# Kernel optimization log

Hardware: AMD Instinct MI355X
Metric: run time of the kernel (lower is better)

## Reference

```python
import jax, jax.numpy as jnp
import numpy as np

N_NODES = 50000
N_EDGES = 800000
DIM = 256


def setup_inputs() -> dict:
    key = jax.random.key(0)
    k1, k2, k3, k4 = jax.random.split(key, 4)
    x = jax.random.normal(k1, (N_NODES, DIM), dtype=jnp.float32)
    edge_index = jax.random.randint(k2, (2, N_EDGES), 0, N_NODES, dtype=jnp.int64)
    # GCNConv learned params (glorot-style weight, zero bias like PyG default init)
    W = jax.random.normal(k3, (DIM, DIM), dtype=jnp.float32) * (1.0 / np.sqrt(DIM))
    b = jnp.zeros((DIM,), dtype=jnp.float32)
    return {"x": x, "edge_index": edge_index, "W": W, "b": b}


def reference(x, edge_index, W, b):
    # GNNBlock forward (eval mode: dropout is identity; normalizer=Identity,
    # activation=ReLU, projection=Identity since in_dim==out_dim).
    n = x.shape[0]
    # --- GCNConv with self-loops and symmetric normalization ---
    loop = jnp.arange(n, dtype=edge_index.dtype)
    src = jnp.concatenate([edge_index[0], loop])  # [E+N]
    dst = jnp.concatenate([edge_index[1], loop])  # [E+N]
    ones = jnp.ones(src.shape[0], dtype=x.dtype)
    deg = jax.ops.segment_sum(ones, dst, num_segments=n)  # in-degree incl. self-loop
    dinv = jnp.where(deg > 0, jax.lax.rsqrt(deg), 0.0)
    norm = dinv[src] * dinv[dst]  # [E+N]
    h = x @ W  # transform first (in->out), then aggregate
    msg = h[src] * norm[:, None]  # gather + scale, [E+N, DIM]
    agg = jax.ops.segment_sum(msg, dst, num_segments=n) + b  # scatter-add
    # --- norm (Identity) -> activation (ReLU) -> residual -> dropout (eval) ---
    out = jax.nn.relu(agg) + x
    return out
```

## Files before the change

### kernel.cpp

```cpp
#include <hip/hip_runtime.h>

#define N_NODES 50000
#define DIM 256
#define NBUCK 196
#define BCAP 6144
#define CEDGES 2048
#define MSTRIDE 512
#define APAD 264
#define EPAD 260
#define TROWS 16

typedef __attribute__((ext_vector_type(8))) short bf16x8;
typedef __attribute__((ext_vector_type(4))) float f32x4;
typedef __attribute__((ext_vector_type(2))) float f32x2;
union U16 { uint4 u; bf16x8 s; };

__device__ __forceinline__ unsigned short f2b(float f) {
    unsigned int u = __float_as_uint(f);
    return (unsigned short)((u + 0x7FFFu + ((u >> 16) & 1u)) >> 16);
}

__global__ __launch_bounds__(256) void prep_bin_kernel(const int* __restrict__ src,
                                                       const int* __restrict__ dst, int E,
                                                       int nCoarse,
                                                       unsigned int* __restrict__ slab2,
                                                       int* __restrict__ meta_t,
                                                       const float* __restrict__ W,
                                                       uint4* __restrict__ Bpack,
                                                       const float* __restrict__ x,
                                                       unsigned int* __restrict__ xq) {
    __shared__ int hist[NBUCK];
    __shared__ int scn[NBUCK];
    __shared__ int cur[NBUCK];
    __shared__ int s2[256];
    __shared__ unsigned int sorted[CEDGES];

    const int tid = threadIdx.x;

    if (blockIdx.x >= (unsigned)nCoarse) {
        int role = blockIdx.x - nCoarse;
        if (role < 32) {
            int gid  = role * 256 + tid;
            int lane = gid & 63;
            int u    = (gid >> 6) & 15;
            int ki   = gid >> 10;
            int n    = u * 16 + (lane & 15);
            int k0   = ki * 32 + (lane >> 4) * 8;
            unsigned int w[4];
            #pragma unroll
            for (int p = 0; p < 4; ++p) {
                unsigned int lo = f2b(W[(size_t)(k0 + 2 * p) * DIM + n]);
                unsigned int hi = f2b(W[(size_t)(k0 + 2 * p + 1) * DIM + n]);
                w[p] = lo | (hi << 16);
            }
            Bpack[gid] = make_uint4(w[0], w[1], w[2], w[3]);
        } else {
            int gid = (role - 32) * 256 + tid;
            float4 v = ((const float4*)x)[gid];
            int p = __builtin_amdgcn_cvt_pk_fp8_f32(v.x, v.y, 0, false);
            p     = __builtin_amdgcn_cvt_pk_fp8_f32(v.z, v.w, p, true);
            xq[gid] = (unsigned int)p;
        }
        return;
    }

    const int e0 = blockIdx.x * CEDGES;
    const int nE = min(CEDGES, E - e0);

    if (tid < NBUCK) hist[tid] = 0;
    __syncthreads();

    unsigned int pk[8];
    #pragma unroll
    for (int i = 0; i < 8; ++i) {
        int idx = i * 256 + tid;
        pk[i] = 0xFFFFFFFFu;
        if (idx < nE) {
            unsigned int s = (unsigned int)src[e0 + idx];
            unsigned int d = (unsigned int)dst[e0 + idx];
            pk[i] = (d << 16) | s;
            atomicAdd(&hist[d >> 8], 1);
        }
    }
    __syncthreads();

    int v = (tid < NBUCK) ? hist[tid] : 0;
    s2[tid] = v;
    __syncthreads();
    for (int off = 1; off < 256; off <<= 1) {
        int t = (tid >= off) ? s2[tid - off] : 0;
        __syncthreads();
        s2[tid] += t;
        __syncthreads();
    }
    if (tid < NBUCK) {
        scn[tid] = s2[tid] - v;
        cur[tid] = 0;
    }
    __syncthreads();

    #pragma unroll
    for (int i = 0; i < 8; ++i) {
        if (pk[i] != 0xFFFFFFFFu) {
            int bkt = pk[i] >> 24;
            int p = scn[bkt] + atomicAdd(&cur[bkt], 1);
            sorted[p] = pk[i];
        }
    }
    __syncthreads();

    for (int i = tid; i < nE; i += 256)
        slab2[(size_t)blockIdx.x * CEDGES + i] = sorted[i];
    if (tid < NBUCK)
        meta_t[tid * MSTRIDE + blockIdx.x] = (scn[tid] << 16) | (hist[tid] & 0xFFFF);
}

__global__ __launch_bounds__(256) void fine_kernel(int nCoarse,
                                                   const unsigned int* __restrict__ slab2,
                                                   const int* __restrict__ meta_t,
                                                   int* __restrict__ offs,
                                                   int* __restrict__ deg,
                                                   float* __restrict__ dinv,
                                                   int* __restrict__ csr_src) {
    __shared__ int rcnt[512];
    __shared__ int rst[512];
    __shared__ int rbase[512];
    __shared__ int scn[256];
    __shared__ int hist[256];
    __shared__ unsigned short rmap[BCAP];
    __shared__ unsigned int stage[BCAP];

    const int tid = threadIdx.x;
    const int g = blockIdx.x;

    for (int b = tid; b < nCoarse; b += 256) {
        int m = meta_t[g * MSTRIDE + b];
        rcnt[b] = m & 0xFFFF;
        rst[b]  = (m >> 16) & 0xFFFF;
    }
    for (int b = nCoarse + tid; b < 512; b += 256) rcnt[b] = 0;
    __syncthreads();

    int c0 = rcnt[2 * tid];
    int c1 = rcnt[2 * tid + 1];
    int ps = c0 + c1;
    scn[tid] = ps;
    __syncthreads();
    for (int off = 1; off < 256; off <<= 1) {
        int t = (tid >= off) ? scn[tid - off] : 0;
        __syncthreads();
        scn[tid] += t;
        __syncthreads();
    }
    int pexcl = scn[tid] - ps;
    rbase[2 * tid]     = pexcl;
    rbase[2 * tid + 1] = pexcl + c0;
    const int total = scn[255];
    hist[tid] = 0;
    __syncthreads();

    #pragma unroll
    for (int rr = 0; rr < 2; ++rr) {
        int r = 2 * tid + rr;
        int n = rcnt[r], b0 = rbase[r];
        for (int k = 0; k < n; ++k)
            if (b0 + k < BCAP) rmap[b0 + k] = (unsigned short)r;
    }
    __syncthreads();

    const int cnt = min(total, BCAP);

    for (int e = tid; e < cnt; e += 256) {
        int r = rmap[e];
        unsigned int p = slab2[(size_t)r * CEDGES + rst[r] + (e - rbase[r])];
        stage[e] = p;
        atomicAdd(&hist[(p >> 16) & 255], 1);
    }
    __syncthreads();

    int d = hist[tid];
    scn[tid] = d;
    __syncthreads();
    for (int off = 1; off < 256; off <<= 1) {
        int t = (tid >= off) ? scn[tid - off] : 0;
        __syncthreads();
        scn[tid] += t;
        __syncthreads();
    }
    int excl = scn[tid] - d;

    int node = g * 256 + tid;
    const int base = g * BCAP;
    if (node < N_NODES) {
        offs[node] = base + excl;
        deg[node]  = d;
        dinv[node] = rsqrtf((float)(d + 1));
    }
    hist[tid] = excl;
    __syncthreads();

    for (int e = tid; e < cnt; e += 256) {
        unsigned int p = stage[e];
        int pos = atomicAdd(&hist[(p >> 16) & 255], 1);
        csr_src[base + pos] = (int)(p & 0xFFFFu);
    }
}

__global__ __launch_bounds__(256) void agg_gemm_kernel(const unsigned int* __restrict__ xq,
                                                       const int* __restrict__ offs,
                                                       const int* __restrict__ deg,
                                                       const int* __restrict__ csr_src,
                                                       const float* __restrict__ dinv,
                                                       const float* __restrict__ x,
                                                       const uint4* __restrict__ Bpack,
                                                       const float* __restrict__ b,
                                                       float* __restrict__ out) {
    __shared__ __align__(16) char LDSraw[TROWS * EPAD * 4];
    ushort* ALDS = (ushort*)LDSraw;
    float*  ELDS = (float*)LDSraw;

    const int tid  = threadIdx.x;
    const int wave = tid >> 6;
    const int lane = tid & 63;
    const int half = lane >> 5;
    const int hl   = lane & 31;
    const int row0 = blockIdx.x * TROWS;
    const uint2* xq2 = (const uint2*)xq;

    for (int j = 0; j < 4; ++j) {
        const int r   = wave * 4 + j;
        const int row = row0 + r;
        if (row < N_NODES) {
            const float di = dinv[row];
            float ac[8];
            {
                uint2 qs = xq2[(size_t)row * 32 + hl];
                float sd = (half == 0) ? di : 0.f;
                f32x2 l0 = __builtin_amdgcn_cvt_pk_f32_fp8((int)qs.x, false);
                f32x2 h0 = __builtin_amdgcn_cvt_pk_f32_fp8((int)qs.x, true);
                f32x2 l1 = __builtin_amdgcn_cvt_pk_f32_fp8((int)qs.y, false);
                f32x2 h1 = __builtin_amdgcn_cvt_pk_f32_fp8((int)qs.y, true);
                ac[0] = l0.x * sd; ac[1] = l0.y * sd; ac[2] = h0.x * sd; ac[3] = h0.y * sd;
                ac[4] = l1.x * sd; ac[5] = l1.y * sd; ac[6] = h1.x * sd; ac[7] = h1.y * sd;
            }

            const int start = offs[row];
            const int n     = deg[row];
            int i = 0;
            for (; i + 16 <= n; i += 16) {
                int   sA[8];
                uint2 qA[8];
                float dA[8];
                #pragma unroll
                for (int u = 0; u < 8; ++u) sA[u] = csr_src[start + i + 2 * u + half];
                #pragma unroll
                for (int u = 0; u < 8; ++u) qA[u] = xq2[(size_t)sA[u] * 32 + hl];
                #pragma unroll
                for (int u = 0; u < 8; ++u) dA[u] = dinv[sA[u]];
                #pragma unroll
                for (int u = 0; u < 8; ++u) {
                    f32x2 l0 = __builtin_amdgcn_cvt_pk_f32_fp8((int)qA[u].x, false);
                    f32x2 h0 = __builtin_amdgcn_cvt_pk_f32_fp8((int)qA[u].x, true);
                    f32x2 l1 = __builtin_amdgcn_cvt_pk_f32_fp8((int)qA[u].y, false);
                    f32x2 h1 = __builtin_amdgcn_cvt_pk_f32_fp8((int)qA[u].y, true);
                    float dd = dA[u];
                    ac[0] += l0.x * dd; ac[1] += l0.y * dd; ac[2] += h0.x * dd; ac[3] += h0.y * dd;
                    ac[4] += l1.x * dd; ac[5] += l1.y * dd; ac[6] += h1.x * dd; ac[7] += h1.y * dd;
                }
            }
            for (; i < n; i += 2) {
                bool valid = (i + half) < n;
                int s = valid ? csr_src[start + i + half] : 0;
                float dd = valid ? dinv[s] : 0.f;
                uint2 q = xq2[(size_t)s * 32 + hl];
                f32x2 l0 = __builtin_amdgcn_cvt_pk_f32_fp8((int)q.x, false);
                f32x2 h0 = __builtin_amdgcn_cvt_pk_f32_fp8((int)q.x, true);
                f32x2 l1 = __builtin_amdgcn_cvt_pk_f32_fp8((int)q.y, false);
                f32x2 h1 = __builtin_amdgcn_cvt_pk_f32_fp8((int)q.y, true);
                ac[0] += l0.x * dd; ac[1] += l0.y * dd; ac[2] += h0.x * dd; ac[3] += h0.y * dd;
                ac[4] += l1.x * dd; ac[5] += l1.y * dd; ac[6] += h1.x * dd; ac[7] += h1.y * dd;
            }

            #pragma unroll
            for (int k = 0; k < 8; ++k) ac[k] = (ac[k] + __shfl_xor(ac[k], 32)) * di;
            unsigned int u0 = (unsigned int)f2b(ac[0]) | ((unsigned int)f2b(ac[1]) << 16);
            unsigned int u1 = (unsigned int)f2b(ac[2]) | ((unsigned int)f2b(ac[3]) << 16);
            unsigned int u2 = (unsigned int)f2b(ac[4]) | ((unsigned int)f2b(ac[5]) << 16);
            unsigned int u3 = (unsigned int)f2b(ac[6]) | ((unsigned int)f2b(ac[7]) << 16);
            if (half == 0)
                *(uint4*)&ALDS[r * APAD + hl * 8] = make_uint4(u0, u1, u2, u3);
        } else if (half == 0) {
            *(uint4*)&ALDS[r * APAD + hl * 8] = make_uint4(0, 0, 0, 0);
        }
    }
    __syncthreads();

    const int m  = lane & 15;
    const int kb = lane >> 4;

    f32x4 acc[4];
    #pragma unroll
    for (int t = 0; t < 4; ++t) acc[t] = (f32x4){0.f, 0.f, 0.f, 0.f};

    const uint4* bp = Bpack + (size_t)(wave * 4) * 64 + lane;

    for (int ki = 0; ki < 8; ++ki) {
        U16 bf[4], af;
        #pragma unroll
        for (int t = 0; t < 4; ++t) bf[t].u = bp[(size_t)(ki * 16 + t) * 64];
        af.u = *(const uint4*)&ALDS[m * APAD + ki * 32 + kb * 8];
        #pragma unroll
        for (int t = 0; t < 4; ++t)
            acc[t] = __builtin_amdgcn_mfma_f32_16x16x32_bf16(af.s, bf[t].s, acc[t], 0, 0, 0);
    }

    __syncthreads();
    #pragma unroll
    for (int t = 0; t < 4; ++t) {
        #pragma unroll
        for (int reg = 0; reg < 4; ++reg) {
            ELDS[(kb * 4 + reg) * EPAD + wave * 64 + t * 16 + m] = acc[t][reg];
        }
    }
    __syncthreads();

    const float4* x4g = (const float4*)x;
    const float4* b4  = (const float4*)b;
    float4* out4 = (float4*)out;

    #pragma unroll
    for (int j = 0; j < 4; ++j) {
        int idx  = j * 256 + tid;
        int lrow = idx >> 6;
        int c4   = idx & 63;
        int grow = row0 + lrow;
        if (grow < N_NODES) {
            float4 v  = *(const float4*)&ELDS[lrow * EPAD + c4 * 4];
            float4 bb = b4[c4];
            float4 xx = x4g[(size_t)grow * 64 + c4];
            float4 o;
            o.x = fmaxf(v.x + bb.x, 0.f) + xx.x;
            o.y = fmaxf(v.y + bb.y, 0.f) + xx.y;
            o.z = fmaxf(v.z + bb.z, 0.f) + xx.z;
            o.w = fmaxf(v.w + bb.w, 0.f) + xx.w;
            out4[(size_t)grow * 64 + c4] = o;
        }
    }
}

extern "C" void kernel_launch(void* const* d_in, const int* in_sizes, int n_in,
                              void* d_out, int out_size, void* d_ws, size_t ws_size,
                              hipStream_t stream) {
    const float* x  = (const float*)d_in[0];
    const int*   ei = (const int*)d_in[1];
    const float* W  = (const float*)d_in[2];
    const float* b  = (const float*)d_in[3];
    float* out = (float*)d_out;
    const int E = in_sizes[1] / 2;

    char* ws = (char*)d_ws;
    int*          deg     = (int*)(ws);
    int*          offs    = (int*)(ws + 262144);
    float*        dinv    = (float*)(ws + 524288);
    int*          csr_src = (int*)(ws + 786432);
    int*          meta_t  = (int*)(ws + 5767168);
    unsigned int* slab2   = (unsigned int*)(ws + 6291456);
    uint4*        Bpack   = (uint4*)(ws + 9699328);
    unsigned int* xq      = (unsigned int*)(ws + 10485760);

    const int* src = ei;
    const int* dst = ei + E;

    const int nCoarse = (E + CEDGES - 1) / CEDGES;
    const int nXq = (N_NODES * 64) / 256;

    prep_bin_kernel<<<nCoarse + 32 + nXq, 256, 0, stream>>>(src, dst, E, nCoarse,
                                                            slab2, meta_t, W, Bpack, x, xq);
    fine_kernel<<<NBUCK, 256, 0, stream>>>(nCoarse, slab2, meta_t, offs, deg, dinv, csr_src);
    agg_gemm_kernel<<<(N_NODES + TROWS - 1) / TROWS, 256, 0, stream>>>(xq, offs, deg, csr_src,
                                                                       dinv, x, Bpack, b, out);
}
```

Measured before the change: 205.9 us.

## Aggregate four rows concurrently per wave with full-wave per-row gathers

Each wave now gathers neighbor features for its four rows at the same time, with all 64 lanes reading 4 fp8 values (one dword) per neighbor row, instead of processing rows one after another with half-waves splitting the edges. This is meant to put more independent loads in flight, hiding gather latency, and it drops the cross-half shuffle reduction. In exchange, loads become 4-byte per lane instead of 8-byte, register use grows, and rows with fewer edges idle while the wave runs to the highest degree of the four.

```diff
diff --git a/kernel.cpp b/kernel.cpp
--- a/kernel.cpp
+++ b/kernel.cpp
@@ -222,76 +222,67 @@
     const int tid  = threadIdx.x;
     const int wave = tid >> 6;
     const int lane = tid & 63;
-    const int half = lane >> 5;
-    const int hl   = lane & 31;
     const int row0 = blockIdx.x * TROWS;
-    const uint2* xq2 = (const uint2*)xq;
-
+
+    int   startJ[4], nJ[4];
+    float diJ[4];
+    float ac[4][4];
+    #pragma unroll
     for (int j = 0; j < 4; ++j) {
-        const int r   = wave * 4 + j;
-        const int row = row0 + r;
-        if (row < N_NODES) {
-            const float di = dinv[row];
-            float ac[8];
-            {
-                uint2 qs = xq2[(size_t)row * 32 + hl];
-                float sd = (half == 0) ? di : 0.f;
-                f32x2 l0 = __builtin_amdgcn_cvt_pk_f32_fp8((int)qs.x, false);
-                f32x2 h0 = __builtin_amdgcn_cvt_pk_f32_fp8((int)qs.x, true);
-                f32x2 l1 = __builtin_amdgcn_cvt_pk_f32_fp8((int)qs.y, false);
-                f32x2 h1 = __builtin_amdgcn_cvt_pk_f32_fp8((int)qs.y, true);
-                ac[0] = l0.x * sd; ac[1] = l0.y * sd; ac[2] = h0.x * sd; ac[3] = h0.y * sd;
-                ac[4] = l1.x * sd; ac[5] = l1.y * sd; ac[6] = h1.x * sd; ac[7] = h1.y * sd;
+        int row = row0 + wave * 4 + j;
+        bool ok = row < N_NODES;
+        int rr = ok ? row : 0;
+        float di = ok ? dinv[rr] : 0.f;
+        diJ[j]    = di;
+        startJ[j] = offs[rr];
+        nJ[j]     = ok ? deg[rr] : 0;
+        unsigned int qs = xq[(size_t)rr * 64 + lane];
+        f32x2 lo = __builtin_amdgcn_cvt_pk_f32_fp8((int)qs, false);
+        f32x2 hi = __builtin_amdgcn_cvt_pk_f32_fp8((int)qs, true);
+        ac[j][0] = lo.x * di; ac[j][1] = lo.y * di;
+        ac[j][2] = hi.x * di; ac[j][3] = hi.y * di;
+    }
+    const int nmax = max(max(nJ[0], nJ[1]), max(nJ[2], nJ[3]));
+
+    for (int i = 0; i < nmax; i += 4) {
+        int sA[4][4];
+        unsigned int qA[4][4];
+        float dA[4][4];
+        #pragma unroll
+        for (int j = 0; j < 4; ++j)
+            #pragma unroll
+            for (int u = 0; u < 4; ++u)
+                sA[j][u] = ((i + u) < nJ[j]) ? csr_src[startJ[j] + i + u] : 0;
+        #pragma unroll
+        for (int j = 0; j < 4; ++j)
+            #pragma unroll
+            for (int u = 0; u < 4; ++u)
+                qA[j][u] = xq[(size_t)sA[j][u] * 64 + lane];
+        #pragma unroll
+        for (int j = 0; j < 4; ++j)
+            #pragma unroll
+            for (int u = 0; u < 4; ++u)
+                dA[j][u] = ((i + u) < nJ[j]) ? dinv[sA[j][u]] : 0.f;
+        #pragma unroll
+        for (int j = 0; j < 4; ++j) {
+            #pragma unroll
+            for (int u = 0; u < 4; ++u) {
+                f32x2 l = __builtin_amdgcn_cvt_pk_f32_fp8((int)qA[j][u], false);
+                f32x2 h = __builtin_amdgcn_cvt_pk_f32_fp8((int)qA[j][u], true);
+                float dd = dA[j][u];
+                ac[j][0] += l.x * dd; ac[j][1] += l.y * dd;
+                ac[j][2] += h.x * dd; ac[j][3] += h.y * dd;
             }
-
-            const int start = offs[row];
-            const int n     = deg[row];
-            int i = 0;
-            for (; i + 16 <= n; i += 16) {
-                int   sA[8];
-                uint2 qA[8];
-                float dA[8];
-                #pragma unroll
-                for (int u = 0; u < 8; ++u) sA[u] = csr_src[start + i + 2 * u + half];
-                #pragma unroll
-                for (int u = 0; u < 8; ++u) qA[u] = xq2[(size_t)sA[u] * 32 + hl];
-                #pragma unroll
-                for (int u = 0; u < 8; ++u) dA[u] = dinv[sA[u]];
-                #pragma unroll
-                for (int u = 0; u < 8; ++u) {
-                    f32x2 l0 = __builtin_amdgcn_cvt_pk_f32_fp8((int)qA[u].x, false);
-                    f32x2 h0 = __builtin_amdgcn_cvt_pk_f32_fp8((int)qA[u].x, true);
-                    f32x2 l1 = __builtin_amdgcn_cvt_pk_f32_fp8((int)qA[u].y, false);
-                    f32x2 h1 = __builtin_amdgcn_cvt_pk_f32_fp8((int)qA[u].y, true);
-                    float dd = dA[u];
-                    ac[0] += l0.x * dd; ac[1] += l0.y * dd; ac[2] += h0.x * dd; ac[3] += h0.y * dd;
-                    ac[4] += l1.x * dd; ac[5] += l1.y * dd; ac[6] += h1.x * dd; ac[7] += h1.y * dd;
-                }
-            }
-            for (; i < n; i += 2) {
-                bool valid = (i + half) < n;
-                int s = valid ? csr_src[start + i + half] : 0;
-                float dd = valid ? dinv[s] : 0.f;
-                uint2 q = xq2[(size_t)s * 32 + hl];
-                f32x2 l0 = __builtin_amdgcn_cvt_pk_f32_fp8((int)q.x, false);
-                f32x2 h0 = __builtin_amdgcn_cvt_pk_f32_fp8((int)q.x, true);
-                f32x2 l1 = __builtin_amdgcn_cvt_pk_f32_fp8((int)q.y, false);
-                f32x2 h1 = __builtin_amdgcn_cvt_pk_f32_fp8((int)q.y, true);
-                ac[0] += l0.x * dd; ac[1] += l0.y * dd; ac[2] += h0.x * dd; ac[3] += h0.y * dd;
-                ac[4] += l1.x * dd; ac[5] += l1.y * dd; ac[6] += h1.x * dd; ac[7] += h1.y * dd;
-            }
-
-            #pragma unroll
-            for (int k = 0; k < 8; ++k) ac[k] = (ac[k] + __shfl_xor(ac[k], 32)) * di;
-            unsigned int u0 = (unsigned int)f2b(ac[0]) | ((unsigned int)f2b(ac[1]) << 16);
-            unsigned int u1 = (unsigned int)f2b(ac[2]) | ((unsigned int)f2b(ac[3]) << 16);
-            unsigned int u2 = (unsigned int)f2b(ac[4]) | ((unsigned int)f2b(ac[5]) << 16);
-            unsigned int u3 = (unsigned int)f2b(ac[6]) | ((unsigned int)f2b(ac[7]) << 16);
-            if (half == 0)
-                *(uint4*)&ALDS[r * APAD + hl * 8] = make_uint4(u0, u1, u2, u3);
-        } else if (half == 0) {
-            *(uint4*)&ALDS[r * APAD + hl * 8] = make_uint4(0, 0, 0, 0);
-        }
+        }
+    }
+
+    #pragma unroll
+    for (int j = 0; j < 4; ++j) {
+        int r = wave * 4 + j;
+        float di = diJ[j];
+        ushort4 st4 = make_ushort4(f2b(ac[j][0] * di), f2b(ac[j][1] * di),
+                                   f2b(ac[j][2] * di), f2b(ac[j][3] * di));
+        *(ushort4*)&ALDS[r * APAD + lane * 4] = st4;
     }
     __syncthreads();
 
```

After: 215.4 us. 1.05x slower.
